# Kernel optimization log

Hardware: AMD Instinct MI355X
Metric: run time of the kernel (lower is better)

Reference implementation:

```python
import jax, jax.numpy as jnp
import numpy as np
import math

B = 1; SEQ = 2048; CHUNK = 16; K = SEQ // CHUNK
DIM = 1024; NH = 16; HD = DIM // NH
NL = 2; NLF = 2; HID = 4096; VOCAB = 32000; CSP_MAX = 4
EPS = 1e-5
BS = CHUNK + 2                 # per-chunk decoder block: [fx, sep, tokens]
L = K * BS + 2                 # + trailing [fx_last, sep]


def rope_cache(n_pos, n_elem, base=10000.0):
    theta = 1.0 / (base ** (jnp.arange(0, n_elem, 2, dtype=jnp.float32) / n_elem))
    idx = jnp.outer(jnp.arange(n_pos, dtype=jnp.float32), theta)  # [n_pos, n_elem/2]
    cos = jnp.concatenate([jnp.cos(idx), jnp.cos(idx)], -1)
    sin = jnp.concatenate([jnp.sin(idx), jnp.sin(idx)], -1)
    return cos, sin  # [n_pos, n_elem]


def apply_rope(x, cos, sin):
    # x: [b, h, l, d]; cos/sin: [l, d] (rope_n_elem == head_dim)
    h = x.shape[-1] // 2
    rot = jnp.concatenate([-x[..., h:], x[..., :h]], -1)
    return x * cos + rot * sin


def rmsnorm(x, w):
    return x * jax.lax.rsqrt(jnp.mean(x * x, -1, keepdims=True) + EPS) * w


def attention(x, wqkv, wo, cos, sin, mask):
    b, l, d = x.shape
    qkv = (x @ wqkv).reshape(b, l, 3, NH, HD).transpose(2, 0, 3, 1, 4)
    q, k, v = qkv[0], qkv[1], qkv[2]            # [b, h, l, hd]
    q = apply_rope(q, cos, sin)
    k = apply_rope(k, cos, sin)
    s = jnp.einsum('bhqd,bhkd->bhqk', q, k) / math.sqrt(HD)
    if mask is not None:
        s = jnp.where(mask, s, jnp.float32(-1e30))
    o = jnp.einsum('bhqk,bhkd->bhqd', jax.nn.softmax(s, -1), v)
    return o.transpose(0, 2, 1, 3).reshape(b, l, d) @ wo


def block(x, ln1, wqkv, wo, ln2, wg, wu, wd, cos, sin, mask):
    x = x + attention(rmsnorm(x, ln1), wqkv, wo, cos, sin, mask)
    h = rmsnorm(x, ln2)
    return x + (jax.nn.silu(h @ wg) * (h @ wu)) @ wd


def cat_mask(n, bs):
    # CAT mask: (kv divides block-start | same block) & causal
    q = jnp.arange(n)[:, None]
    kv = jnp.arange(n)[None, :]
    return ((kv % bs == 0) | (q // bs == kv // bs)) & (q >= kv)


def setup_inputs() -> dict:
    key = jax.random.key(0)
    ks = jax.random.split(key, 24)
    w = lambda k, s: jax.random.normal(k, s, jnp.float32) * 0.02
    return {
        'input_ids': jax.random.randint(ks[0], (B, SEQ), 0, VOCAB, dtype=jnp.int32),
        'chunk_size_power': 4,
        'f_wte': w(ks[1], (VOCAB, DIM)), 'f_pos': w(ks[2], (SEQ, DIM)),
        'f_adapt': w(ks[3], (CSP_MAX + 1, DIM)),
        'f_ln1': jnp.ones((NLF, DIM)), 'f_ln2': jnp.ones((NLF, DIM)),
        'f_wqkv': w(ks[4], (NLF, DIM, 3 * DIM)), 'f_wo': w(ks[5], (NLF, DIM, DIM)),
        'f_wg': w(ks[6], (NLF, DIM, HID)), 'f_wu': w(ks[7], (NLF, DIM, HID)),
        'f_wd': w(ks[8], (NLF, HID, DIM)),
        'f_norm': jnp.ones((DIM,)), 'f_proj': w(ks[9], (DIM, CHUNK * DIM)),
        'dummy_fx': w(ks[10], (CSP_MAX + 1, DIM)), 'wte': w(ks[11], (VOCAB, DIM)),
        'sep': w(ks[12], (1, DIM)),
        'd_ln1': jnp.ones((NL, DIM)), 'd_ln2': jnp.ones((NL, DIM)),
        'd_wqkv': w(ks[13], (NL, DIM, 3 * DIM)), 'd_wo': w(ks[14], (NL, DIM, DIM)),
        'd_wg': w(ks[15], (NL, DIM, HID)), 'd_wu': w(ks[16], (NL, DIM, HID)),
        'd_wd': w(ks[17], (NL, HID, DIM)),
        'd_norm': jnp.ones((DIM,)), 'w_out': w(ks[18], (VOCAB, DIM)),
    }


def reference(input_ids, chunk_size_power, f_wte, f_pos, f_adapt, f_ln1, f_ln2,
              f_wqkv, f_wo, f_wg, f_wu, f_wd, f_norm, f_proj, dummy_fx, wte, sep,
              d_ln1, d_ln2, d_wqkv, d_wo, d_wg, d_wu, d_wd, d_norm, w_out):
    csp = int(chunk_size_power)
    ids = input_ids.reshape(B, K, CHUNK)
    cosf, sinf = rope_cache(2 + CHUNK, HD)

    def compress(ids_c, chunk_idx):
        # ids_c: [B, CHUNK] (one chunk, vmapped over K)
        x = f_wte[ids_c]
        adaptive = jnp.broadcast_to(f_adapt[csp], (B, 1, DIM))
        pos_tok = jnp.broadcast_to(f_pos[chunk_idx], (B, 1, DIM))
        x = jnp.concatenate([adaptive, pos_tok, x], 1)  # [B, CHUNK+2, DIM]
        for i in range(NLF):
            x = block(x, f_ln1[i], f_wqkv[i], f_wo[i], f_ln2[i],
                      f_wg[i], f_wu[i], f_wd[i], cosf, sinf, None)
        x = rmsnorm(x, f_norm)[:, 2:, :].reshape(B, CHUNK * DIM)
        # chunk_size_power == log2(CHUNK): bilinear interpolate to same size == identity
        return x @ f_proj.T  # [B, DIM]

    fx = jax.vmap(compress, in_axes=(1, 0), out_axes=1)(ids, jnp.arange(K))  # [B, K, DIM]

    fx_last = fx[:, -1:, :]
    dummy = jnp.broadcast_to(dummy_fx[csp], (B, 1, DIM))
    fx_sh = jnp.concatenate([dummy, fx[:, :-1, :]], 1)[:, :, None, :]  # [B, K, 1, DIM]
    sep_t = jnp.broadcast_to(sep[0], (B, K, 1, DIM))
    emb = wte[ids]  # [B, K, CHUNK, DIM]
    x = jnp.concatenate([fx_sh, sep_t, emb], 2).reshape(B, K * BS, DIM)
    x = jnp.concatenate([x, fx_last, jnp.broadcast_to(sep[0], (B, 1, DIM))], 1)  # [B, L, DIM]

    # per-block repeating RoPE positions (cache built for len BS, tiled)
    pos = jnp.tile(jnp.arange(BS), K + 1)[:L]
    cosb, sinb = rope_cache(BS, HD)
    cosd, sind = cosb[pos], sinb[pos]
    mask = cat_mask(L, BS)

    for i in range(NL):
        x = block(x, d_ln1[i], d_wqkv[i], d_wo[i], d_ln2[i],
                  d_wg[i], d_wu[i], d_wd[i], cosd, sind, mask)
    x = rmsnorm(x, d_norm)
    return x @ w_out.T  # [B, L, VOCAB]
```

## Files before the change

kernel.cpp:

```cpp
#include <hip/hip_runtime.h>
#include <math.h>

#define L_DEC 2306
#define MPAD 2560
#define T_FINE 2304

typedef float f32x4 __attribute__((ext_vector_type(4)));
typedef __bf16 bf16x8 __attribute__((ext_vector_type(8)));
typedef unsigned short u16;
typedef unsigned short us4 __attribute__((ext_vector_type(4)));
typedef unsigned short us8 __attribute__((ext_vector_type(8)));

#define GLOAD16(g, l) __builtin_amdgcn_global_load_lds( \
    (const __attribute__((address_space(1))) unsigned int*)(g), \
    (__attribute__((address_space(3))) unsigned int*)(l), 16, 0, 0)

__device__ __forceinline__ u16 f2bf(float f) {
  unsigned u = __float_as_uint(f);
  u += 0x7fffu + ((u >> 16) & 1u);
  return (u16)(u >> 16);
}

__device__ __forceinline__ int fix_csp(const int* p) {
  int c = p[0];
  if ((unsigned)c <= 4u) return c;
  float f = __uint_as_float((unsigned)c);
  int c2 = (int)f;
  return ((unsigned)c2 <= 4u) ? c2 : 4;
}

__device__ __forceinline__ void xcd_map(int gx, int gy, int& bm, int& bn, int TS) {
  const int nwg = gx * gy;
  const int orig = blockIdx.y * gx + blockIdx.x;
  const int q8 = nwg >> 3, r8 = nwg & 7;
  const int xcd = orig & 7, idx8 = orig >> 3;
  const int wg = (xcd < r8 ? xcd * (q8 + 1) : r8 * (q8 + 1) + (xcd - r8) * q8) + idx8;
  bm = (wg / gx) * TS;
  bn = (wg % gx) * TS;
}

template<int EPI>
__global__ __launch_bounds__(512, 1) void k_gemm3(const u16* __restrict__ A,
                                                  const u16* __restrict__ B,
                                                  float* __restrict__ C,
                                                  int N, int K, int Mstore)
{
  extern __shared__ u16 lds[];
  const int tid = threadIdx.x;
  int bm, bn; xcd_map(gridDim.x, gridDim.y, bm, bn, 256);
  const int w = tid >> 6, lane = tid & 63;
  const int wm = (w >> 2) * 128, wn = (w & 3) * 64;
  const int lr = lane & 15, kh = lane >> 4;

#define STAGE3(buf, kt) do {                                                   \
    u16* lA = lds + (buf) * 32768;                                             \
    u16* lB = lA + 16384;                                                      \
    _Pragma("unroll")                                                          \
    for (int p = 0; p < 4; ++p) {                                              \
      int e = p * 512 + tid;                                                   \
      int row = e >> 3;                                                        \
      int kc = ((e & 7) ^ (row & 7)) * 8;    \
      GLOAD16(A + (size_t)(bm + row) * K + (size_t)(kt) * 64 + kc, lA + e * 8);\
      GLOAD16(B + (size_t)(bn + row) * K + (size_t)(kt) * 64 + kc, lB + e * 8);\
    }                                                                          \
  } while (0)

  f32x4 acc[8][4] = {};
  const int nt = K >> 6;
  STAGE3(0, 0);
  int cur = 0;
  for (int t = 0; t < nt; ++t) {
    if (t + 1 < nt) {
      STAGE3(cur ^ 1, t + 1);
      asm volatile("s_waitcnt vmcnt(8)" ::: "memory");
    } else {
      asm volatile("s_waitcnt vmcnt(0)" ::: "memory");
    }
    __builtin_amdgcn_s_barrier();
    asm volatile("" ::: "memory");
    const u16* pA = lds + cur * 32768;
    const u16* pB = pA + 16384;
    const int xr = (lr & 7) << 3;
#pragma unroll
    for (int kt2 = 0; kt2 < 2; ++kt2) {
      bf16x8 af[8], bf[4];
#pragma unroll
      for (int m = 0; m < 8; ++m)
        af[m] = *(const bf16x8*)&pA[(wm + m * 16 + lr) * 64 + ((kt2 * 32 + kh * 8) ^ xr)];
#pragma unroll
      for (int n = 0; n < 4; ++n)
        bf[n] = *(const bf16x8*)&pB[(wn + n * 16 + lr) * 64 + ((kt2 * 32 + kh * 8) ^ xr)];
#pragma unroll
      for (int m = 0; m < 8; ++m)
#pragma unroll
        for (int n = 0; n < 4; ++n)
          acc[m][n] = __builtin_amdgcn_mfma_f32_16x16x32_bf16(af[m], bf[n], acc[m][n], 0, 0, 0);
    }
    asm volatile("" ::: "memory");
    __builtin_amdgcn_s_barrier();
    cur ^= 1;
  }
#undef STAGE3

#pragma unroll
  for (int m = 0; m < 8; ++m) {
    int gr0 = bm + wm + m * 16 + kh * 4;
#pragma unroll
    for (int n = 0; n < 4; ++n) {
      int gc = bn + wn + n * 16 + lr;
#pragma unroll
      for (int r = 0; r < 4; ++r) {
        int gr = gr0 + r;
        if (gr < Mstore) C[(size_t)gr * N + gc] = acc[m][n][r];
      }
    }
  }
}

template<int EPI>
__global__ __launch_bounds__(512, 1) void k_gemm2(const u16* __restrict__ A,
                                                  const u16* __restrict__ B,
                                                  float* __restrict__ C,
                                                  u16* __restrict__ Cb,
                                                  int N, int K, int Mstore)
{
  __shared__ u16 As[2][8192];
  __shared__ u16 Bs[2][8192];
  const int tid = threadIdx.x;
  int bm, bn; xcd_map(gridDim.x, gridDim.y, bm, bn, 256);
  const int w = tid >> 6, lane = tid & 63;
  const int wm = (w >> 2) * 128, wn = (w & 3) * 64;
  const int lr = lane & 15, kh = lane >> 4;
  const int r0 = tid >> 2;
  const int ksrc = 8 * ((tid & 3) ^ ((tid >> 3) & 3));
  const u16* ga = A + (size_t)(bm + r0) * K + ksrc;
  const u16* gb = B + (size_t)(bn + r0) * K + ksrc;
  const size_t rstep = (size_t)128 * K;
  const int cola = (kh * 8) ^ (((lr >> 1) & 3) << 3);

#define STAGE2(buf, kt) do {                                   \
    const u16* gA = ga + (size_t)(kt) * 32;                    \
    const u16* gB = gb + (size_t)(kt) * 32;                    \
    GLOAD16(gA,         &As[buf][tid * 8]);                    \
    GLOAD16(gA + rstep, &As[buf][tid * 8 + 4096]);             \
    GLOAD16(gB,         &Bs[buf][tid * 8]);                    \
    GLOAD16(gB + rstep, &Bs[buf][tid * 8 + 4096]);             \
  } while (0)

  f32x4 acc[8][4] = {};
  const int nt = K >> 5;
  STAGE2(0, 0);
  __syncthreads();
  int cur = 0;
  for (int t = 0; t < nt; ++t) {
    if (t + 1 < nt) STAGE2(cur ^ 1, t + 1);
    bf16x8 af[8], bf[4];
#pragma unroll
    for (int m = 0; m < 8; ++m)
      af[m] = *(const bf16x8*)&As[cur][(wm + m * 16 + lr) * 32 + cola];
#pragma unroll
    for (int n = 0; n < 4; ++n)
      bf[n] = *(const bf16x8*)&Bs[cur][(wn + n * 16 + lr) * 32 + cola];
#pragma unroll
    for (int m = 0; m < 8; ++m)
#pragma unroll
      for (int n = 0; n < 4; ++n)
        acc[m][n] = __builtin_amdgcn_mfma_f32_16x16x32_bf16(af[m], bf[n], acc[m][n], 0, 0, 0);
    __syncthreads();
    cur ^= 1;
  }
#undef STAGE2

#pragma unroll
  for (int m = 0; m < 8; ++m) {
    int gr0 = bm + wm + m * 16 + kh * 4;
#pragma unroll
    for (int n = 0; n < 4; ++n) {
      int gc = bn + wn + n * 16 + lr;
#pragma unroll
      for (int r = 0; r < 4; ++r) {
        int gr = gr0 + r;
        if (gr < Mstore) C[(size_t)gr * N + gc] = acc[m][n][r];
      }
    }
  }
}

template<int EPI>
__global__ __launch_bounds__(256) void k_gemm_bt(const u16* __restrict__ A,
                                                 const u16* __restrict__ B,
                                                 float* __restrict__ C,
                                                 u16* __restrict__ Cb,
                                                 const float* __restrict__ cosT,
                                                 const float* __restrict__ sinT,
                                                 int N, int K, int Mstore, int kchunk)
{
  __shared__ u16 ldsAB[2][16384];
  const int tid = threadIdx.x;
  int bm, bn; xcd_map(gridDim.x, gridDim.y, bm, bn, 128);
  const int k0 = blockIdx.z * kchunk;
  const int w = tid >> 6, lane = tid & 63;
  const int wm = (w >> 1) * 64, wn = (w & 1) * 64;
  const int lr = lane & 15, kh = lane >> 4;

#define STAGE4(buf, kt) do {                                                       \
    u16* lA = &ldsAB[buf][0];                                                      \
    u16* lB = &ldsAB[buf][8192];                                                   \
    _Pragma("unroll")                                                              \
    for (int p = 0; p < 4; ++p) {                                                  \
      int e = p * 256 + tid;                                                       \
      int row = e >> 3;                                                            \
      int kc = ((e & 7) ^ (row & 7)) * 8;                                          \
      GLOAD16(A + (size_t)(bm + row) * K + k0 + (size_t)(kt) * 64 + kc, lA + e * 8);\
      GLOAD16(B + (size_t)(bn + row) * K + k0 + (size_t)(kt) * 64 + kc, lB + e * 8);\
    }                                                                              \
  } while (0)

  f32x4 acc[4][4] = {};
  const int nt = kchunk >> 6;
  STAGE4(0, 0);
  int cur = 0;
  for (int t = 0; t < nt; ++t) {
    if (t + 1 < nt) {
      STAGE4(cur ^ 1, t + 1);
      asm volatile("s_waitcnt vmcnt(8)" ::: "memory");
    } else {
      asm volatile("s_waitcnt vmcnt(0)" ::: "memory");
    }
    __builtin_amdgcn_s_barrier();
    asm volatile("" ::: "memory");
    const u16* pA = &ldsAB[cur][0];
    const u16* pB = &ldsAB[cur][8192];
    const int xr = (lr & 7) << 3;
#pragma unroll
    for (int kt2 = 0; kt2 < 2; ++kt2) {
      bf16x8 af[4], bfr[4];
#pragma unroll
      for (int m = 0; m < 4; ++m)
        af[m] = *(const bf16x8*)&pA[(wm + m * 16 + lr) * 64 + ((kt2 * 32 + kh * 8) ^ xr)];
#pragma unroll
      for (int n = 0; n < 4; ++n)
        bfr[n] = *(const bf16x8*)&pB[(wn + n * 16 + lr) * 64 + ((kt2 * 32 + kh * 8) ^ xr)];
#pragma unroll
      for (int m = 0; m < 4; ++m)
#pragma unroll
        for (int n = 0; n < 4; ++n)
          acc[m][n] = __builtin_amdgcn_mfma_f32_16x16x32_bf16(af[m], bfr[n], acc[m][n], 0, 0, 0);
    }
    asm volatile("" ::: "memory");
    __builtin_amdgcn_s_barrier();
    cur ^= 1;
  }
#undef STAGE4

  float* Cz = (EPI == 0) ? C + (size_t)blockIdx.z * Mstore * N : C;
  const int N2 = N >> 1;
  const bool doRope = (EPI == 3) && ((bn + wn) < 2048);
#pragma unroll
  for (int m = 0; m < 4; ++m) {
    int gr0 = bm + wm + m * 16 + kh * 4;
#pragma unroll
    for (int r = 0; r < 4; ++r) {
      int gr = gr0 + r;
      if (EPI == 3) {
        int p = gr % 18;
        if (doRope) {
#pragma unroll
          for (int n2 = 0; n2 < 2; ++n2) {
            int d = n2 * 16 + lr;
            float c = cosT[p * 64 + d], s = sinT[p * 64 + d];
            float x1 = acc[m][n2][r], x2 = acc[m][n2 + 2][r];
            if (gr < Mstore) {
              int gc = bn + wn + n2 * 16 + lr;
              C[(size_t)gr * N + gc]      = x1 * c - x2 * s;
              C[(size_t)gr * N + gc + 32] = x2 * c + x1 * s;
            }
          }
        } else if (gr < Mstore) {
#pragma unroll
          for (int n = 0; n < 4; ++n)
            C[(size_t)gr * N + bn + wn + n * 16 + lr] = acc[m][n][r];
        }
      } else if (EPI == 2) {
#pragma unroll
        for (int n = 0; n < 4; ++n) {
          float x = acc[m][n][r];
          float px = __shfl_xor(x, 1);
          if (!(lr & 1) && gr < Mstore) {
            int gc = bn + wn + n * 16 + lr;
            float sgl = x / (1.f + expf(-x)) * px;
            Cb[(size_t)gr * N2 + (gc >> 1)] = f2bf(sgl);
          }
        }
      } else {
        if (gr < Mstore) {
#pragma unroll
          for (int n = 0; n < 4; ++n)
            Cz[(size_t)gr * N + bn + wn + n * 16 + lr] = acc[m][n][r];
        }
      }
    }
  }
}

__global__ __launch_bounds__(256) void k_gemm_hf(const u16* __restrict__ A,
                                                 const float* __restrict__ B,
                                                 float* __restrict__ C,
                                                 int N, int K, int Mstore)
{
  __shared__ u16 As[4096];
  __shared__ u16 Bs[4096];
  const int tid = threadIdx.x;
  const int bm = blockIdx.y * 128, bn = blockIdx.x * 128;
  const int w = tid >> 6, lane = tid & 63;
  const int wm = (w >> 1) * 64, wn = (w & 1) * 64;
  const int lr = lane & 15, kh = lane >> 4;
  const int r0 = tid >> 2;
  const int ksrc = 8 * ((tid & 3) ^ ((tid >> 3) & 3));
  const int cola = (kh * 8) ^ (((lr >> 1) & 3) << 3);
  const u16* ga = A + (size_t)(bm + r0) * K + ksrc;
  u16* la = &As[tid * 8];
  const size_t rstep = (size_t)64 * K;

  f32x4 acc[4][4] = {};
  for (int kk = 0; kk < K; kk += 32) {
    GLOAD16(ga, la); GLOAD16(ga + rstep, la + 2048);
    ga += 32;
#pragma unroll
    for (int p = 0; p < 4; ++p) {
      int e = tid + p * 256;
      int row = e >> 3, kc = (e & 7) * 4;
      int kcs = kc ^ (((row >> 1) & 3) << 3);
      float4 v = *(const float4*)(B + (size_t)(bn + row) * K + kk + kc);
      us4 pk; pk[0] = f2bf(v.x); pk[1] = f2bf(v.y); pk[2] = f2bf(v.z); pk[3] = f2bf(v.w);
      *(us4*)&Bs[row * 32 + kcs] = pk;
    }
    __syncthreads();
    bf16x8 af[4], bfr[4];
#pragma unroll
    for (int m = 0; m < 4; ++m)
      af[m] = *(const bf16x8*)&As[(wm + m * 16 + lr) * 32 + cola];
#pragma unroll
    for (int n = 0; n < 4; ++n)
      bfr[n] = *(const bf16x8*)&Bs[(wn + n * 16 + lr) * 32 + cola];
#pragma unroll
    for (int m = 0; m < 4; ++m)
#pragma unroll
      for (int n = 0; n < 4; ++n)
        acc[m][n] = __builtin_amdgcn_mfma_f32_16x16x32_bf16(af[m], bfr[n], acc[m][n], 0, 0, 0);
    __syncthreads();
  }
#pragma unroll
  for (int m = 0; m < 4; ++m) {
    int gr0 = bm + wm + m * 16 + kh * 4;
#pragma unroll
    for (int n = 0; n < 4; ++n) {
      int gc = bn + wn + n * 16 + lr;
#pragma unroll
      for (int r = 0; r < 4; ++r) {
        int gr = gr0 + r;
        if (gr < Mstore) C[(size_t)gr * N + gc] = acc[m][n][r];
      }
    }
  }
}

__global__ __launch_bounds__(256) void k_wt2(const float* __restrict__ W,
                                             const float* __restrict__ W2,
                                             u16* __restrict__ Wt,
                                             int K, int N, int rs, int ro) {
  __shared__ u16 t[64][80];
  const float* src = (blockIdx.z == 0) ? W : W2;
  int roz = ro + blockIdx.z;
  int n0 = blockIdx.x * 64, k0 = blockIdx.y * 64;
#pragma unroll
  for (int p = 0; p < 4; ++p) {
    int id = threadIdx.x + p * 256;
    int row = id >> 4, c4 = (id & 15) * 4;
    float4 v = *(const float4*)(src + (size_t)(k0 + row) * N + n0 + c4);
    t[c4 + 0][row] = f2bf(v.x);
    t[c4 + 1][row] = f2bf(v.y);
    t[c4 + 2][row] = f2bf(v.z);
    t[c4 + 3][row] = f2bf(v.w);
  }
  __syncthreads();
#pragma unroll
  for (int p = 0; p < 2; ++p) {
    int id = threadIdx.x + p * 256;
    int row = id >> 3, c8 = (id & 7) * 8;
    *(us8*)(Wt + ((size_t)(n0 + row) * rs + roz) * K + k0 + c8) = *(const us8*)&t[row][c8];
  }
}

__global__ void k_cvt(const float* __restrict__ x, u16* __restrict__ y, int n4) {
  for (int i = blockIdx.x * 256 + threadIdx.x; i < n4; i += gridDim.x * 256) {
    float4 v = ((const float4*)x)[i];
    us4 p; p[0] = f2bf(v.x); p[1] = f2bf(v.y); p[2] = f2bf(v.z); p[3] = f2bf(v.w);
    ((us4*)y)[i] = p;
  }
}

__global__ void k_reduce_add(const float* __restrict__ p, float* __restrict__ dst,
                             int n, int planes, int addDst) {
  for (int i = blockIdx.x * 256 + threadIdx.x; i < n; i += gridDim.x * 256) {
    float s = addDst ? dst[i] : 0.f;
    for (int z = 0; z < planes; ++z) s += p[(size_t)z * n + i];
    dst[i] = s;
  }
}

template<int S, int NORM>
__global__ __launch_bounds__(256) void k_red_norm(const float* __restrict__ planes,
                                                  float* __restrict__ x,
                                                  const float* __restrict__ w,
                                                  u16* __restrict__ y) {
  const int t = blockIdx.x;
  const int n = gridDim.x * 1024;
  const size_t base = (size_t)t * 1024 + threadIdx.x * 4;
  float4 a = *(const float4*)(x + base);
#pragma unroll
  for (int s = 0; s < S; ++s) {
    float4 p = *(const float4*)(planes + (size_t)s * n + base);
    a.x += p.x; a.y += p.y; a.z += p.z; a.w += p.w;
  }
  *(float4*)(x + base) = a;
  if (NORM) {
    float ss = a.x * a.x + a.y * a.y + a.z * a.z + a.w * a.w;
#pragma unroll
    for (int off = 32; off; off >>= 1) ss += __shfl_xor(ss, off);
    __shared__ float ps[4];
    if ((threadIdx.x & 63) == 0) ps[threadIdx.x >> 6] = ss;
    __syncthreads();
    float inv = rsqrtf((ps[0] + ps[1] + ps[2] + ps[3]) * (1.f / 1024.f) + 1e-5f);
    const float4 wv = *(const float4*)(w + threadIdx.x * 4);
    us4 o;
    o[0] = f2bf(a.x * inv * wv.x); o[1] = f2bf(a.y * inv * wv.y);
    o[2] = f2bf(a.z * inv * wv.z); o[3] = f2bf(a.w * inv * wv.w);
    *(us4*)(y + base) = o;
  }
}

__global__ void k_rope_table(float* __restrict__ cosT, float* __restrict__ sinT) {
  int i = blockIdx.x * blockDim.x + threadIdx.x;
  if (i >= 18 * 64) return;
  int p = i >> 6, d = i & 63;
  float theta = powf(10000.f, -(float)(d & 31) / 32.f);
  float ang = (float)p * theta;
  cosT[i] = cosf(ang);
  sinT[i] = sinf(ang);
}

__global__ void k_fine_embed(const int* __restrict__ ids, const int* __restrict__ cspp,
                             const float* __restrict__ f_wte, const float* __restrict__ f_pos,
                             const float* __restrict__ f_adapt, float* __restrict__ xF) {
  int csp = fix_csp(cspp);
  for (int idx = blockIdx.x * 256 + threadIdx.x; idx < T_FINE * 1024; idx += gridDim.x * 256) {
    int r = idx >> 10, d = idx & 1023;
    int c = r / 18, j = r - c * 18;
    float v;
    if (j == 0)      v = f_adapt[csp * 1024 + d];
    else if (j == 1) v = f_pos[c * 1024 + d];
    else             v = f_wte[(size_t)ids[c * 16 + j - 2] * 1024 + d];
    xF[idx] = v;
  }
}

__global__ __launch_bounds__(256) void k_rmsnorm_bf(const float* __restrict__ x,
                                                    const float* __restrict__ w,
                                                    u16* __restrict__ y) {
  int t = blockIdx.x;
  const float4 v = *(const float4*)(x + (size_t)t * 1024 + threadIdx.x * 4);
  float ss = v.x * v.x + v.y * v.y + v.z * v.z + v.w * v.w;
#pragma unroll
  for (int off = 32; off; off >>= 1) ss += __shfl_xor(ss, off);
  __shared__ float ps[4];
  if ((threadIdx.x & 63) == 0) ps[threadIdx.x >> 6] = ss;
  __syncthreads();
  float inv = rsqrtf((ps[0] + ps[1] + ps[2] + ps[3]) * (1.f / 1024.f) + 1e-5f);
  const float4 wv = *(const float4*)(w + threadIdx.x * 4);
  us4 o;
  o[0] = f2bf(v.x * inv * wv.x); o[1] = f2bf(v.y * inv * wv.y);
  o[2] = f2bf(v.z * inv * wv.z); o[3] = f2bf(v.w * inv * wv.w);
  *(us4*)(y + (size_t)t * 1024 + threadIdx.x * 4) = o;
}

__global__ __launch_bounds__(256) void k_rmsnorm_pack_bf(const float* __restrict__ x,
                                                         const float* __restrict__ w,
                                                         u16* __restrict__ y) {
  int b = blockIdx.x;
  int c = b >> 4, r = b & 15;
  const float* xr = x + (size_t)(c * 18 + 2 + r) * 1024;
  const float4 v = *(const float4*)(xr + threadIdx.x * 4);
  float ss = v.x * v.x + v.y * v.y + v.z * v.z + v.w * v.w;
#pragma unroll
  for (int off = 32; off; off >>= 1) ss += __shfl_xor(ss, off);
  __shared__ float ps[4];
  if ((threadIdx.x & 63) == 0) ps[threadIdx.x >> 6] = ss;
  __syncthreads();
  float inv = rsqrtf((ps[0] + ps[1] + ps[2] + ps[3]) * (1.f / 1024.f) + 1e-5f);
  const float4 wv = *(const float4*)(w + threadIdx.x * 4);
  us4 o;
  o[0] = f2bf(v.x * inv * wv.x); o[1] = f2bf(v.y * inv * wv.y);
  o[2] = f2bf(v.z * inv * wv.z); o[3] = f2bf(v.w * inv * wv.w);
  *(us4*)(y + (size_t)b * 1024 + threadIdx.x * 4) = o;
}

__global__ __launch_bounds__(256) void k_attn_fine2(const float* __restrict__ qkv,
                                                    u16* __restrict__ out) {
  __shared__ float q[4][18][68], k[4][18][68], v[4][18][68], s[4][18][20];
  int c = blockIdx.x;
  int w = threadIdx.x >> 6, lane = threadIdx.x & 63;
  int h = blockIdx.y * 4 + w;
  const float* base = qkv + (size_t)c * 18 * 3072 + h * 64;
#pragma unroll 3
  for (int r = 0; r < 18; ++r) {
    q[w][r][lane] = base[(size_t)r * 3072 + lane];
    k[w][r][lane] = base[(size_t)r * 3072 + 1024 + lane];
    v[w][r][lane] = base[(size_t)r * 3072 + 2048 + lane];
  }
  __syncthreads();
#pragma unroll
  for (int it = 0; it < 6; ++it) {
    int idx = lane + it * 64;
    if (idx < 324) {
      int qi = (idx * 3641) >> 16;
      int ki = idx - qi * 18;
      const float* qr = q[w][qi];
      const float* kr = k[w][ki];
      float a = 0.f;
#pragma unroll
      for (int d = 0; d < 64; d += 4) {
        float4 x = *(const float4*)&qr[d];
        float4 y = *(const float4*)&kr[d];
        a += x.x * y.x + x.y * y.y + x.z * y.z + x.w * y.w;
      }
      s[w][qi][ki] = a * 0.125f;
    }
  }
  __syncthreads();
  if (lane < 18) {
    float mx = -1e30f;
#pragma unroll
    for (int j = 0; j < 18; ++j) mx = fmaxf(mx, s[w][lane][j]);
    float sum = 0.f;
#pragma unroll
    for (int j = 0; j < 18; ++j) { float e = expf(s[w][lane][j] - mx); s[w][lane][j] = e; sum += e; }
    float inv = 1.f / sum;
#pragma unroll
    for (int j = 0; j < 18; ++j) s[w][lane][j] *= inv;
  }
  __syncthreads();
  float vcol[18];
#pragma unroll
  for (int ki = 0; ki < 18; ++ki) vcol[ki] = v[w][ki][lane];
#pragma unroll 2
  for (int qi = 0; qi < 18; ++qi) {
    float o = 0.f;
#pragma unroll
    for (int ki = 0; ki < 18; ++ki) o += s[w][qi][ki] * vcol[ki];
    out[(size_t)(c * 18 + qi) * 1024 + h * 64 + lane] = f2bf(o);
  }
}

__global__ __launch_bounds__(512) void k_attn_dec3(const float* __restrict__ qkv,
                                                   u16* __restrict__ out) {
  extern __shared__ float dyn[];
  float* Kl = dyn;
  float* Vl = Kl + 146 * 65;
  float* Ql = Vl + 146 * 65;
  float* Sw = Ql + 18 * 65;
  const int bq = blockIdx.x, h = blockIdx.y;
  const int w = threadIdx.x >> 6, lane = threadIdx.x & 63;
  const int t0 = 18 * bq;
  const int nq = (bq < 128) ? 18 : 2;
  const int nstage = (bq < 128) ? (bq + 18) : 130;

  {
    int rr = threadIdx.x >> 2, c = threadIdx.x & 3;
    for (int row = rr; row < nstage; row += 128) {
      int kv = (row <= bq) ? 18 * row : t0 + (row - bq);
      const float* kp = qkv + (size_t)kv * 3072 + 1024 + h * 64 + c * 16;
#pragma unroll
      for (int q4 = 0; q4 < 4; ++q4) {
        float4 a = *(const float4*)(kp + q4 * 4);
        float4 b = *(const float4*)(kp + 1024 + q4 * 4);
        int d = c * 16 + q4 * 4;
        float* kd = Kl + row * 65 + d;
        float* vd = Vl + row * 65 + d;
        kd[0] = a.x; kd[1] = a.y; kd[2] = a.z; kd[3] = a.w;
        vd[0] = b.x; vd[1] = b.y; vd[2] = b.z; vd[3] = b.w;
      }
    }
    if (rr < nq) {
      const float* qp = qkv + (size_t)(t0 + rr) * 3072 + h * 64 + c * 16;
#pragma unroll
      for (int q4 = 0; q4 < 4; ++q4) {
        float4 a = *(const float4*)(qp + q4 * 4);
        int d = c * 16 + q4 * 4;
        float* qd = Ql + rr * 65 + d;
        qd[0] = a.x; qd[1] = a.y; qd[2] = a.z; qd[3] = a.w;
      }
    }
  }
  __syncthreads();

  for (int r = w; r < nq; r += 8) {
    const int nk = bq + 1 + r;
    float* S = Sw + w * 148;
    const float* qr = Ql + r * 65;
    float mx = -1e30f;
    for (int i = lane; i < nk; i += 64) {
      const float* kr = Kl + i * 65;
      float a = 0.f;
#pragma unroll
      for (int d = 0; d < 64; ++d) a += qr[d] * kr[d];
      a *= 0.125f;
      S[i] = a;
      mx = fmaxf(mx, a);
    }
#pragma unroll
    for (int off = 32; off; off >>= 1) mx = fmaxf(mx, __shfl_xor(mx, off));
    float sum = 0.f;
    for (int i = lane; i < nk; i += 64) { float e = expf(S[i] - mx); S[i] = e; sum += e; }
#pragma unroll
    for (int off = 32; off; off >>= 1) sum += __shfl_xor(sum, off);
    float inv = 1.f / sum;
    __builtin_amdgcn_wave_barrier();
    float o = 0.f;
    for (int i = 0; i < nk; ++i) o += S[i] * Vl[i * 65 + lane];
    out[(size_t)(t0 + r) * 1024 + h * 64 + lane] = f2bf(o * inv);
  }
}

__global__ __launch_bounds__(256) void k_attn_dec2(const float* __restrict__ qkv,
                                                   u16* __restrict__ out) {
  __shared__ float sc_s[4][160];
  int t = blockIdx.x;
  int w = threadIdx.x >> 6, lane = threadIdx.x & 63;
  int h = blockIdx.y * 4 + w;
  float* sc = sc_s[w];
  int bq = t / 18;
  int nstart = bq + 1;
  int nown = t - 18 * bq;
  int nk = nstart + nown;
  int g = lane >> 2, j = lane & 3;
  const float* qb = qkv + (size_t)t * 3072 + h * 64 + j * 16;
  float4 q0 = *(const float4*)(qb);
  float4 q1 = *(const float4*)(qb + 4);
  float4 q2 = *(const float4*)(qb + 8);
  float4 q3 = *(const float4*)(qb + 12);
  for (int i0 = 0; i0 < nk; i0 += 16) {
    int i = i0 + g;
    float p = 0.f;
    if (i < nk) {
      int kv = (i < nstart) ? 18 * i : 18 * bq + (i - nstart) + 1;
      const float* kp = qkv + (size_t)kv * 3072 + 1024 + h * 64 + j * 16;
      float4 k0 = *(const float4*)(kp);
      float4 k1 = *(const float4*)(kp + 4);
      float4 k2 = *(const float4*)(kp + 8);
      float4 k3 = *(const float4*)(kp + 12);
      p = q0.x * k0.x + q0.y * k0.y + q0.z * k0.z + q0.w * k0.w
        + q1.x * k1.x + q1.y * k1.y + q1.z * k1.z + q1.w * k1.w
        + q2.x * k2.x + q2.y * k2.y + q2.z * k2.z + q2.w * k2.w
        + q3.x * k3.x + q3.y * k3.y + q3.z * k3.z + q3.w * k3.w;
    }
    p += __shfl_xor(p, 1);
    p += __shfl_xor(p, 2);
    if (i < nk && j == 0) sc[i] = p * 0.125f;
  }
  __syncthreads();
  float mx = -1e30f;
  for (int i = lane; i < nk; i += 64) mx = fmaxf(mx, sc[i]);
#pragma unroll
  for (int off = 32; off; off >>= 1) mx = fmaxf(mx, __shfl_xor(mx, off));
  float sum = 0.f;
  for (int i = lane; i < nk; i += 64) { float e = expf(sc[i] - mx); sc[i] = e; sum += e; }
#pragma unroll
  for (int off = 32; off; off >>= 1) sum += __shfl_xor(sum, off);
  float inv = 1.f / sum;
  __syncthreads();
  const float* vb = qkv + 2048 + h * 64 + lane;
  float o0 = 0.f, o1 = 0.f, o2 = 0.f, o3 = 0.f;
  int i = 0;
  for (; i + 4 <= nk; i += 4) {
    int ia = i, ib = i + 1, ic = i + 2, id = i + 3;
    int kva = (ia < nstart) ? 18 * ia : 18 * bq + (ia - nstart) + 1;
    int kvb = (ib < nstart) ? 18 * ib : 18 * bq + (ib - nstart) + 1;
    int kvc = (ic < nstart) ? 18 * ic : 18 * bq + (ic - nstart) + 1;
    int kvd = (id < nstart) ? 18 * id : 18 * bq + (id - nstart) + 1;
    o0 += sc[ia] * vb[(size_t)kva * 3072];
    o1 += sc[ib] * vb[(size_t)kvb * 3072];
    o2 += sc[ic] * vb[(size_t)kvc * 3072];
    o3 += sc[id] * vb[(size_t)kvd * 3072];
  }
  for (; i < nk; ++i) {
    int kv = (i < nstart) ? 18 * i : 18 * bq + (i - nstart) + 1;
    o0 += sc[i] * vb[(size_t)kv * 3072];
  }
  float o = (o0 + o1) + (o2 + o3);
  out[(size_t)t * 1024 + h * 64 + lane] = f2bf(o * inv);
}

__global__ void k_assemble(const int* __restrict__ ids, const int* __restrict__ cspp,
                           const float* __restrict__ fx, const float* __restrict__ dummy_fx,
                           const float* __restrict__ sep, const float* __restrict__ wte,
                           float* __restrict__ xD) {
  int csp = fix_csp(cspp);
  for (int idx = blockIdx.x * 256 + threadIdx.x; idx < MPAD * 1024; idx += gridDim.x * 256) {
    int t = idx >> 10, d = idx & 1023;
    float v;
    if (t >= L_DEC)     v = 0.f;
    else if (t == 2305) v = sep[d];
    else if (t == 2304) v = fx[127 * 1024 + d];
    else {
      int k = t / 18, r = t - k * 18;
      if (r == 0)      v = (k == 0) ? dummy_fx[csp * 1024 + d] : fx[(k - 1) * 1024 + d];
      else if (r == 1) v = sep[d];
      else             v = wte[(size_t)ids[k * 16 + r - 2] * 1024 + d];
    }
    xD[idx] = v;
  }
}

extern "C" void kernel_launch(void* const* d_in, const int* in_sizes, int n_in,
                              void* d_out, int out_size, void* d_ws, size_t ws_size,
                              hipStream_t stream) {
  const int*   input_ids = (const int*)d_in[0];
  const int*   cspp      = (const int*)d_in[1];
  const float* f_wte     = (const float*)d_in[2];
  const float* f_pos     = (const float*)d_in[3];
  const float* f_adapt   = (const float*)d_in[4];
  const float* f_ln1     = (const float*)d_in[5];
  const float* f_ln2     = (const float*)d_in[6];
  const float* f_wqkv    = (const float*)d_in[7];
  const float* f_wo      = (const float*)d_in[8];
  const float* f_wg      = (const float*)d_in[9];
  const float* f_wu      = (const float*)d_in[10];
  const float* f_wd      = (const float*)d_in[11];
  const float* f_norm    = (const float*)d_in[12];
  const float* f_proj    = (const float*)d_in[13];
  const float* dummy_fx  = (const float*)d_in[14];
  const float* wte       = (const float*)d_in[15];
  const float* sep       = (const float*)d_in[16];
  const float* d_ln1     = (const float*)d_in[17];
  const float* d_ln2     = (const float*)d_in[18];
  const float* d_wqkv    = (const float*)d_in[19];
  const float* d_wo      = (const float*)d_in[20];
  const float* d_wg      = (const float*)d_in[21];
  const float* d_wu      = (const float*)d_in[22];
  const float* d_wd      = (const float*)d_in[23];
  const float* d_norm    = (const float*)d_in[24];
  const float* w_out     = (const float*)d_in[25];

  float* cosT = (float*)d_ws;
  float* sinT = cosT + 1152;
  u16*   bufH = (u16*)(sinT + 1152);
  u16*   w_outb = bufH + (size_t)MPAD * 1024;
  const size_t WS_NEED = 2 * 1152 * 4 + (size_t)MPAD * 1024 * 2 + (size_t)32000 * 1024 * 2;
  const bool big_ws = ws_size >= WS_NEED;

  float* o       = (float*)d_out;
  float* xF      = o;
  float* xD      = xF + (size_t)T_FINE * 1024;
  float* fx      = xD + (size_t)MPAD * 1024;
  float* bufQKV  = fx + 128 * 1024;
  u16*   bufA    = (u16*)(bufQKV + (size_t)MPAD * 3072);
  u16*   bufGb   = bufA + (size_t)MPAD * 1024;
  u16*   packedb = bufGb + (size_t)MPAD * 4096;
  u16*   Wt      = packedb + (size_t)128 * 16384;
  u16*   projb   = Wt + (size_t)8192 * 1024;
  float* spk     = (float*)(projb + (size_t)1024 * 16384);

  const size_t ATTN_LDS = (size_t)(146 * 65 * 2 + 18 * 65 + 8 * 148) * 4;
  hipError_t eattn = hipFuncSetAttribute(
      reinterpret_cast<const void*>(&k_attn_dec3),
      hipFuncAttributeMaxDynamicSharedMemorySize, (int)ATTN_LDS);

#define GEMM_BT(EPI, Ap, Bp, Cp, Cbp, Mpad, N, K, Mstore, S) \
  k_gemm_bt<EPI><<<dim3((N) / 128, (Mpad) / 128, (S)), 256, 0, stream>>>((Ap), (Bp), (Cp), (Cbp), cosT, sinT, (N), (K), (Mstore), (K) / (S))
#define WT1(Wp, Kd, Nd) k_wt2<<<dim3((Nd) / 64, (Kd) / 64, 1), 256, 0, stream>>>((Wp), nullptr, Wt, (Kd), (Nd), 1, 0)

  k_rope_table<<<5, 256, 0, stream>>>(cosT, sinT);
  k_fine_embed<<<2048, 256, 0, stream>>>(input_ids, cspp, f_wte, f_pos, f_adapt, xF);
  k_rmsnorm_bf<<<T_FINE, 256, 0, stream>>>(xF, f_ln1, bufH);

  for (int i = 0; i < 2; ++i) {
    WT1(f_wqkv + (size_t)i * 1024 * 3072, 1024, 3072);
    GEMM_BT(3, bufH, Wt, bufQKV, (u16*)nullptr, T_FINE, 3072, 1024, T_FINE, 1);
    k_attn_fine2<<<dim3(128, 4), 256, 0, stream>>>(bufQKV, bufA);
    WT1(f_wo + (size_t)i * 1024 * 1024, 1024, 1024);
    GEMM_BT(0, bufA, Wt, spk, (u16*)nullptr, T_FINE, 1024, 1024, T_FINE, 2);
    k_red_norm<2, 1><<<T_FINE, 256, 0, stream>>>(spk, xF, f_ln2 + i * 1024, bufH);
    k_wt2<<<dim3(64, 16, 2), 256, 0, stream>>>(f_wg + (size_t)i * 1024 * 4096,
                                               f_wu + (size_t)i * 1024 * 4096, Wt, 1024, 4096, 2, 0);
    GEMM_BT(2, bufH, Wt, (float*)nullptr, bufGb, T_FINE, 8192, 1024, T_FINE, 1);
    WT1(f_wd + (size_t)i * 4096 * 1024, 4096, 1024);
    GEMM_BT(0, bufGb, Wt, spk, (u16*)nullptr, T_FINE, 1024, 4096, T_FINE, 4);
    if (i == 0) k_red_norm<4, 1><<<T_FINE, 256, 0, stream>>>(spk, xF, f_ln1 + 1024, bufH);
    else        k_red_norm<4, 0><<<T_FINE, 256, 0, stream>>>(spk, xF, nullptr, nullptr);
  }

  k_rmsnorm_pack_bf<<<2048, 256, 0, stream>>>(xF, f_norm, packedb);
  k_cvt<<<2048, 256, 0, stream>>>(f_proj, projb, 1024 * 16384 / 4);
  GEMM_BT(0, packedb, projb, spk, (u16*)nullptr, 128, 1024, 16384, 128, 32);
  k_reduce_add<<<512, 256, 0, stream>>>(spk, fx, 128 * 1024, 32, 0);

  k_assemble<<<2048, 256, 0, stream>>>(input_ids, cspp, fx, dummy_fx, sep, wte, xD);
  k_rmsnorm_bf<<<MPAD, 256, 0, stream>>>(xD, d_ln1, bufH);
  for (int i = 0; i < 2; ++i) {
    WT1(d_wqkv + (size_t)i * 1024 * 3072, 1024, 3072);
    GEMM_BT(3, bufH, Wt, bufQKV, (u16*)nullptr, MPAD, 3072, 1024, MPAD, 1);
    if (eattn == hipSuccess) {
      k_attn_dec3<<<dim3(129, 16), 512, ATTN_LDS, stream>>>(bufQKV, bufA);
    } else {
      k_attn_dec2<<<dim3(L_DEC, 4), 256, 0, stream>>>(bufQKV, bufA);
    }
    WT1(d_wo + (size_t)i * 1024 * 1024, 1024, 1024);
    GEMM_BT(0, bufA, Wt, spk, (u16*)nullptr, MPAD, 1024, 1024, MPAD, 2);
    k_red_norm<2, 1><<<MPAD, 256, 0, stream>>>(spk, xD, d_ln2 + i * 1024, bufH);
    k_wt2<<<dim3(64, 16, 2), 256, 0, stream>>>(d_wg + (size_t)i * 1024 * 4096,
                                               d_wu + (size_t)i * 1024 * 4096, Wt, 1024, 4096, 2, 0);
    GEMM_BT(2, bufH, Wt, (float*)nullptr, bufGb, MPAD, 8192, 1024, MPAD, 1);
    WT1(d_wd + (size_t)i * 4096 * 1024, 4096, 1024);
    GEMM_BT(0, bufGb, Wt, spk, (u16*)nullptr, MPAD, 1024, 4096, MPAD, 4);
    const float* nw = (i == 0) ? d_ln1 + 1024 : d_norm;
    k_red_norm<4, 1><<<MPAD, 256, 0, stream>>>(spk, xD, nw, bufH);
  }

  if (big_ws) {
    k_cvt<<<2048, 256, 0, stream>>>(w_out, w_outb, 32000 * 1024 / 4);
    hipError_t ae = hipFuncSetAttribute(
        reinterpret_cast<const void*>(&k_gemm3<0>),
        hipFuncAttributeMaxDynamicSharedMemorySize, 131072);
    if (ae == hipSuccess) {
      k_gemm3<0><<<dim3(125, 10), 512, 131072, stream>>>(bufH, w_outb, o, 32000, 1024, L_DEC);
    } else {
      k_gemm2<0><<<dim3(125, 10), 512, 0, stream>>>(bufH, w_outb, o, nullptr, 32000, 1024, L_DEC);
    }
  } else {
    k_gemm_hf<<<dim3(250, MPAD / 128), 256, 0, stream>>>(bufH, w_out, o, 32000, 1024, L_DEC);
  }
#undef WT1
#undef GEMM_BT
}
```

Before: 1.273 ms.

## Make output-projection GEMM persistent over M tiles per workgroup

Adds k_gemm3p, a variant of the 256x256 bf16 MFMA GEMM where each workgroup iterates over 5 consecutive M tiles for a fixed N tile. The vocab projection now launches a 125x2 grid instead of 125x10, so 250 workgroups roughly fill the CUs in a single wave instead of 1250 workgroups spread over several waves. The B (weight) tile column stays hot in cache across the M loop. The risk is that the XCD-aware remapping is dropped, fewer workgroups give less latency hiding, and the epilogue stores are no longer overlapped with the next tile's loads.

```diff
diff --git a/kernel.cpp b/kernel.cpp
--- a/kernel.cpp
+++ b/kernel.cpp
@@ -37,6 +37,85 @@
   const int wg = (xcd < r8 ? xcd * (q8 + 1) : r8 * (q8 + 1) + (xcd - r8) * q8) + idx8;
   bm = (wg / gx) * TS;
   bn = (wg % gx) * TS;
+}
+
+__global__ __launch_bounds__(512, 1) void k_gemm3p(const u16* __restrict__ A,
+                                                   const u16* __restrict__ B,
+                                                   float* __restrict__ C,
+                                                   int N, int K, int Mstore, int MT)
+{
+  extern __shared__ u16 lds[];
+  const int tid = threadIdx.x;
+  const int bn = blockIdx.x * 256;
+  const int w = tid >> 6, lane = tid & 63;
+  const int wm = (w >> 2) * 128, wn = (w & 3) * 64;
+  const int lr = lane & 15, kh = lane >> 4;
+  const int nt = K >> 6;
+
+#define STAGE3(buf, kt, bmv) do {                                              \
+    u16* lA = lds + (buf) * 32768;                                             \
+    u16* lB = lA + 16384;                                                      \
+    _Pragma("unroll")                                                          \
+    for (int p = 0; p < 4; ++p) {                                              \
+      int e = p * 512 + tid;                                                   \
+      int row = e >> 3;                                                        \
+      int kc = ((e & 7) ^ (row & 7)) * 8;    \
+      GLOAD16(A + (size_t)((bmv) + row) * K + (size_t)(kt) * 64 + kc, lA + e * 8);\
+      GLOAD16(B + (size_t)(bn + row) * K + (size_t)(kt) * 64 + kc, lB + e * 8);\
+    }                                                                          \
+  } while (0)
+
+  for (int mt = 0; mt < MT; ++mt) {
+    const int bm = (blockIdx.y * MT + mt) * 256;
+    f32x4 acc[8][4] = {};
+    STAGE3(0, 0, bm);
+    int cur = 0;
+    for (int t = 0; t < nt; ++t) {
+      if (t + 1 < nt) {
+        STAGE3(cur ^ 1, t + 1, bm);
+        asm volatile("s_waitcnt vmcnt(8)" ::: "memory");
+      } else {
+        asm volatile("s_waitcnt vmcnt(0)" ::: "memory");
+      }
+      __builtin_amdgcn_s_barrier();
+      asm volatile("" ::: "memory");
+      const u16* pA = lds + cur * 32768;
+      const u16* pB = pA + 16384;
+      const int xr = (lr & 7) << 3;
+#pragma unroll
+      for (int kt2 = 0; kt2 < 2; ++kt2) {
+        bf16x8 af[8], bf[4];
+#pragma unroll
+        for (int m = 0; m < 8; ++m)
+          af[m] = *(const bf16x8*)&pA[(wm + m * 16 + lr) * 64 + ((kt2 * 32 + kh * 8) ^ xr)];
+#pragma unroll
+        for (int n = 0; n < 4; ++n)
+          bf[n] = *(const bf16x8*)&pB[(wn + n * 16 + lr) * 64 + ((kt2 * 32 + kh * 8) ^ xr)];
+#pragma unroll
+        for (int m = 0; m < 8; ++m)
+#pragma unroll
+          for (int n = 0; n < 4; ++n)
+            acc[m][n] = __builtin_amdgcn_mfma_f32_16x16x32_bf16(af[m], bf[n], acc[m][n], 0, 0, 0);
+      }
+      asm volatile("" ::: "memory");
+      __builtin_amdgcn_s_barrier();
+      cur ^= 1;
+    }
+#pragma unroll
+    for (int m = 0; m < 8; ++m) {
+      int gr0 = bm + wm + m * 16 + kh * 4;
+#pragma unroll
+      for (int n = 0; n < 4; ++n) {
+        int gc = bn + wn + n * 16 + lr;
+#pragma unroll
+        for (int r = 0; r < 4; ++r) {
+          int gr = gr0 + r;
+          if (gr < Mstore) C[(size_t)gr * N + gc] = acc[m][n][r];
+        }
+      }
+    }
+  }
+#undef STAGE3
 }
 
 template<int EPI>
@@ -59,7 +138,7 @@
     for (int p = 0; p < 4; ++p) {                                              \
       int e = p * 512 + tid;                                                   \
       int row = e >> 3;                                                        \
-      int kc = ((e & 7) ^ (row & 7)) * 8;    \
+      int kc = ((e & 7) ^ (row & 7)) * 8;                                      \
       GLOAD16(A + (size_t)(bm + row) * K + (size_t)(kt) * 64 + kc, lA + e * 8);\
       GLOAD16(B + (size_t)(bn + row) * K + (size_t)(kt) * 64 + kc, lB + e * 8);\
     }                                                                          \
@@ -830,10 +909,10 @@
   if (big_ws) {
     k_cvt<<<2048, 256, 0, stream>>>(w_out, w_outb, 32000 * 1024 / 4);
     hipError_t ae = hipFuncSetAttribute(
-        reinterpret_cast<const void*>(&k_gemm3<0>),
+        reinterpret_cast<const void*>(&k_gemm3p),
         hipFuncAttributeMaxDynamicSharedMemorySize, 131072);
     if (ae == hipSuccess) {
-      k_gemm3<0><<<dim3(125, 10), 512, 131072, stream>>>(bufH, w_outb, o, 32000, 1024, L_DEC);
+      k_gemm3p<<<dim3(125, 2), 512, 131072, stream>>>(bufH, w_outb, o, 32000, 1024, L_DEC, 5);
     } else {
       k_gemm2<0><<<dim3(125, 10), 512, 0, stream>>>(bufH, w_outb, o, nullptr, 32000, 1024, L_DEC);
     }
```

New measurement: 1.286 ms. Within noise of the previous version (+1.1%).
